# Kernel optimization log

Measured on AMD Instinct MI355X. Metric: run time of the kernel, lower is better.

## Reference

```python
import jax, jax.numpy as jnp
import numpy as np

BN_EPS = 1e-5

def _batchnorm(h, gamma, beta):
    # PyTorch BatchNorm1d in training mode: biased batch statistics over dim 0
    mu = jnp.mean(h, axis=0)
    var = jnp.mean((h - mu) ** 2, axis=0)
    return (h - mu) * jax.lax.rsqrt(var + BN_EPS) * gamma + beta


def setup_inputs() -> dict:
    key = jax.random.key(0)
    ks = jax.random.split(key, 8)
    N, E, D = 50000, 800000, 128
    x = jax.random.normal(ks[0], (N, D), dtype=jnp.float32)
    edge_index = jax.random.randint(ks[1], (2, E), 0, N, dtype=jnp.int64)
    s1 = 1.0 / np.sqrt(D)
    W1 = jax.random.uniform(ks[2], (D, D), jnp.float32, -s1, s1)
    b1 = jax.random.uniform(ks[3], (D,), jnp.float32, -s1, s1)
    W2 = jax.random.uniform(ks[4], (D, D), jnp.float32, -s1, s1)
    b2 = jax.random.uniform(ks[5], (D,), jnp.float32, -s1, s1)
    g1 = jnp.ones((D,), jnp.float32); beta1 = jnp.zeros((D,), jnp.float32)
    g2 = jnp.ones((D,), jnp.float32); beta2 = jnp.zeros((D,), jnp.float32)
    eps = jnp.array([0.1], jnp.float32)
    return {"x": x, "edge_index": edge_index, "eps": eps,
            "W1": W1, "b1": b1, "g1": g1, "beta1": beta1,
            "W2": W2, "b2": b2, "g2": g2, "beta2": beta2}


def reference(x, edge_index, eps, W1, b1, g1, beta1, W2, b2, g2, beta2):
    src, dst = edge_index[0], edge_index[1]
    N = x.shape[0]
    # gather by src, scatter-add to dst
    aggr = jax.ops.segment_sum(x[src], dst, num_segments=N)
    out = (1.0 + eps) * x + aggr  # eps broadcast (shape [1])
    h = jax.nn.relu(_batchnorm(out @ W1 + b1, g1, beta1))
    h = jax.nn.relu(_batchnorm(h @ W2 + b2, g2, beta2))
    return h
```

## Files before the change

### kernel.cpp

```cpp
#include <hip/hip_runtime.h>

#define D 128
#define FB 4096
#define GCAP 1024

typedef __attribute__((ext_vector_type(8))) short short8;
typedef __attribute__((ext_vector_type(4))) float f32x4;

static __device__ __forceinline__ unsigned short f2bf(float f) {
    union { float f; unsigned u; } v; v.f = f;
    unsigned r = v.u + 0x7FFF + ((v.u >> 16) & 1);
    return (unsigned short)(r >> 16);
}

static __device__ __forceinline__ float2 bfpair2f(unsigned p) {
    union { unsigned u; float f; } a, b;
    a.u = (p & 0xFFFFu) << 16;
    b.u = p & 0xFFFF0000u;
    return make_float2(a.f, b.f);
}

__global__ __launch_bounds__(256) void prep_kernel(
    const float4* __restrict__ x4, uint2* __restrict__ xh, int xtotal,
    const float* __restrict__ W1, const float* __restrict__ W2,
    unsigned short* __restrict__ Wf1, unsigned short* __restrict__ Wf2,
    float* __restrict__ stats, int* __restrict__ bucketCount,
    int* __restrict__ bar, unsigned short* __restrict__ zrow, int xblocks)
{
    if (blockIdx.x < (unsigned)xblocks) {
        int i = blockIdx.x * 256 + threadIdx.x;
        if (i >= xtotal) return;
        float4 v = x4[i];
        uint2 o;
        o.x = (unsigned)f2bf(v.x) | ((unsigned)f2bf(v.y) << 16);
        o.y = (unsigned)f2bf(v.z) | ((unsigned)f2bf(v.w) << 16);
        xh[i] = o;
    } else if (blockIdx.x < (unsigned)(xblocks + 128)) {
        int idx = (blockIdx.x - xblocks) * 256 + threadIdx.x;
        const float* W = (idx < 16384) ? W1 : W2;
        unsigned short* Wf = (idx < 16384) ? Wf1 : Wf2;
        int e = idx & 16383;
        int j = e & 7, lane = (e >> 3) & 63, ckk = e >> 9;
        int ct = ckk & 7, kk = ckk >> 3;
        int k = kk * 32 + (lane >> 4) * 8 + j;
        int n = ct * 16 + (lane & 15);
        Wf[e] = f2bf(W[k * 128 + n]);
    } else {
        int t = threadIdx.x;
        stats[t] = 0.f; stats[t + 256] = 0.f;
        bucketCount[t] = 0; bucketCount[t + 256] = 0;
        if (t < 128) zrow[t] = 0;
        if (t < 4) bar[t] = 0;
    }
}

__global__ __launch_bounds__(256) void bucket_hist_kernel(
    const int* __restrict__ ei, int E, int NB, int* __restrict__ bucketCount)
{
    __shared__ int hist[512];
    int tid = threadIdx.x;
    for (int i = tid; i < NB; i += 256) hist[i] = 0;
    __syncthreads();
    int b0 = blockIdx.x * FB;
    int lim = min(FB, E - b0);
    for (int i = tid; i < lim; i += 256)
        atomicAdd(&hist[ei[E + b0 + i] >> 7], 1);
    __syncthreads();
    for (int i = tid; i < NB; i += 256)
        if (hist[i]) atomicAdd(&bucketCount[i], hist[i]);
}

__global__ __launch_bounds__(256) void scanfill_kernel(
    const int* __restrict__ ei, int E, int NB,
    const int* __restrict__ bucketCount,
    int* __restrict__ bucketBase, int* __restrict__ bucketCursor,
    int* __restrict__ flag, unsigned* __restrict__ rec)
{
    int tid = threadIdx.x;
    if (blockIdx.x == 0) {
        __shared__ int sm[256];
        int i0 = 2 * tid, i1 = 2 * tid + 1;
        int c0 = (i0 < NB) ? bucketCount[i0] : 0;
        int c1 = (i1 < NB) ? bucketCount[i1] : 0;
        int t = c0 + c1;
        sm[tid] = t;
        __syncthreads();
        #pragma unroll
        for (int off = 1; off < 256; off <<= 1) {
            int u = (tid >= off) ? sm[tid - off] : 0;
            __syncthreads();
            sm[tid] += u;
            __syncthreads();
        }
        int ex = sm[tid] - t;
        if (i0 < NB) { bucketBase[i0] = ex;      bucketCursor[i0] = ex; }
        if (i1 < NB) { bucketBase[i1] = ex + c0; bucketCursor[i1] = ex + c0; }
        if (tid == 0) bucketBase[NB] = E;
        __threadfence();
        __syncthreads();
        if (tid == 0)
            __hip_atomic_store(flag, 1, __ATOMIC_RELEASE, __HIP_MEMORY_SCOPE_AGENT);
    } else {
        __shared__ int hist[512], base[512];
        int b0 = (blockIdx.x - 1) * FB;
        for (int i = tid; i < NB; i += 256) hist[i] = 0;
        __syncthreads();
        int lim = min(FB, E - b0);
        for (int i = tid; i < lim; i += 256)
            atomicAdd(&hist[ei[E + b0 + i] >> 7], 1);
        __syncthreads();
        if (tid == 0) {
            while (__hip_atomic_load(flag, __ATOMIC_ACQUIRE, __HIP_MEMORY_SCOPE_AGENT) == 0)
                __builtin_amdgcn_s_sleep(2);
        }
        __syncthreads();
        for (int i = tid; i < NB; i += 256) {
            int c = hist[i];
            base[i] = c ? atomicAdd(&bucketCursor[i], c) : 0;
            hist[i] = 0;
        }
        __syncthreads();
        for (int i = tid; i < lim; i += 256) {
            int e = b0 + i;
            int dst = ei[E + e], src = ei[e];
            int bk = dst >> 7;
            int r = atomicAdd(&hist[bk], 1);
            rec[base[bk] + r] = ((unsigned)src << 7) | (unsigned)(dst & 127);
        }
    }
}

__global__ __launch_bounds__(256) void bucket_gather_kernel(
    const unsigned* __restrict__ xh, const unsigned* __restrict__ rec,
    const int* __restrict__ bucketBase, const float* __restrict__ epsp,
    unsigned* __restrict__ h0, int N, int zrow)
{
    int bk = blockIdx.x >> 2;
    int sub = blockIdx.x & 3;
    int tid = threadIdx.x;
    int d0 = (bk << 7) + (sub << 5);

    __shared__ int cnts[32], rnk[32], offs[33];
    __shared__ int slist[GCAP];

    if (tid < 32) { cnts[tid] = 0; rnk[tid] = 0; }
    __syncthreads();

    int lo = bucketBase[bk], hi = bucketBase[bk + 1];
    for (int i = lo + tid; i < hi; i += 256) {
        unsigned r = rec[i];
        int dl = r & 127;
        if ((dl >> 5) == sub) atomicAdd(&cnts[dl & 31], 1);
    }
    __syncthreads();
    if (tid == 0) {
        int run = 0;
        #pragma unroll
        for (int i = 0; i < 32; ++i) { offs[i] = run; run += cnts[i]; }
        offs[32] = run;
    }
    __syncthreads();
    for (int i = lo + tid; i < hi; i += 256) {
        unsigned r = rec[i];
        int dl = r & 127;
        if ((dl >> 5) == sub) {
            int d5 = dl & 31;
            int rk = atomicAdd(&rnk[d5], 1);
            int pos = offs[d5] + rk;
            if (pos < GCAP) slist[pos] = (int)(r >> 7);
        }
    }
    __syncthreads();

    int wv = tid >> 6, lane = tid & 63;
    float epsv = 1.0f + __ldg(epsp);

    #pragma unroll 1
    for (int jj = 0; jj < 4; ++jj) {
        int dA = d0 + wv * 8 + jj * 2;
        int dB = dA + 1;
        int vA = (dA < N), vB = (dB < N);
        int iA = offs[(dA - d0)];
        int eA = offs[(dA - d0) + 1];
        int iB = vB ? offs[(dB - d0)] : 0;
        int eB = vB ? offs[(dB - d0) + 1] : 0;
        if (iA > GCAP) iA = GCAP;
        if (eA > GCAP) eA = GCAP;
        if (iB > GCAP) iB = GCAP;
        if (eB > GCAP) eB = GCAP;
        if (!vA) { iA = 0; eA = 0; }

        float2 xvA = bfpair2f(xh[(size_t)(vA ? dA : 0) * 64 + lane]);
        float2 xvB = bfpair2f(xh[(size_t)(vB ? dB : 0) * 64 + lane]);
        float axA = epsv * xvA.x, ayA = epsv * xvA.y;
        float axB = epsv * xvB.x, ayB = epsv * xvB.y;

        int iters = (eA - iA) > (eB - iB) ? (eA - iA) : (eB - iB);
        for (int it = 0; it < iters; it += 8) {
            unsigned pvA[8], pvB[8];
            #pragma unroll
            for (int k = 0; k < 8; ++k) {
                int idxA = (iA + k < eA) ? slist[iA + k] : zrow;
                int idxB = (iB + k < eB) ? slist[iB + k] : zrow;
                pvA[k] = xh[(size_t)idxA * 64 + lane];
                pvB[k] = xh[(size_t)idxB * 64 + lane];
            }
            #pragma unroll
            for (int k = 0; k < 8; ++k) {
                float2 a = bfpair2f(pvA[k]);
                float2 b = bfpair2f(pvB[k]);
                axA += a.x; ayA += a.y;
                axB += b.x; ayB += b.y;
            }
            iA += 8; iB += 8;
        }
        if (vA) h0[(size_t)dA * 64 + lane] =
            (unsigned)f2bf(axA) | ((unsigned)f2bf(ayA) << 16);
        if (vB) h0[(size_t)dB * 64 + lane] =
            (unsigned)f2bf(axB) | ((unsigned)f2bf(ayB) << 16);
    }
}

__global__ __launch_bounds__(256) void gemm_bn_mfma_kernel(
    const unsigned short* __restrict__ a_bf,
    const float* __restrict__ stat_in, const float* __restrict__ gamma,
    const float* __restrict__ beta, float invN,
    const unsigned short* __restrict__ Wf, const float* __restrict__ bias,
    unsigned short* __restrict__ zout,
    float* __restrict__ stat_sum, float* __restrict__ stat_sq,
    int N, int mode)
{
    __shared__ unsigned short Wl[16384];
    __shared__ float part[1024];
    __shared__ float scf[128], shf[128];

    int tid = threadIdx.x;
    {
        float4* dst = (float4*)Wl;
        const float4* srcp = (const float4*)Wf;
        #pragma unroll
        for (int i = 0; i < 8; ++i) dst[tid + i * 256] = srcp[tid + i * 256];
    }
    if (mode == 1 && tid < 128) {
        float mean = stat_in[tid] * invN;
        float var  = stat_in[128 + tid] * invN - mean * mean;
        float sv = gamma[tid] * rsqrtf(var + 1e-5f);
        scf[tid] = sv;
        shf[tid] = fmaf(-mean, sv, beta[tid]);
    }
    __syncthreads();

    int w = tid >> 6, lane = tid & 63, q = lane >> 4, n16 = lane & 15;
    int rowb = blockIdx.x * 64 + w * 16;
    int m = rowb + n16;
    int mc = (m < N) ? m : (N - 1);
    const unsigned short* arow = a_bf + (size_t)mc * D;

    f32x4 acc[8];
    #pragma unroll
    for (int ct = 0; ct < 8; ++ct) acc[ct] = (f32x4){0.f, 0.f, 0.f, 0.f};

    #pragma unroll
    for (int kk = 0; kk < 4; ++kk) {
        int c = kk * 32 + q * 8;
        short8 af;
        if (mode == 0) {
            af = *(const short8*)(arow + c);
        } else {
            uint4 rw = *(const uint4*)(arow + c);
            float2 p0 = bfpair2f(rw.x), p1 = bfpair2f(rw.y);
            float2 p2 = bfpair2f(rw.z), p3 = bfpair2f(rw.w);
            p0.x = fmaxf(fmaf(p0.x, scf[c + 0], shf[c + 0]), 0.f);
            p0.y = fmaxf(fmaf(p0.y, scf[c + 1], shf[c + 1]), 0.f);
            p1.x = fmaxf(fmaf(p1.x, scf[c + 2], shf[c + 2]), 0.f);
            p1.y = fmaxf(fmaf(p1.y, scf[c + 3], shf[c + 3]), 0.f);
            p2.x = fmaxf(fmaf(p2.x, scf[c + 4], shf[c + 4]), 0.f);
            p2.y = fmaxf(fmaf(p2.y, scf[c + 5], shf[c + 5]), 0.f);
            p3.x = fmaxf(fmaf(p3.x, scf[c + 6], shf[c + 6]), 0.f);
            p3.y = fmaxf(fmaf(p3.y, scf[c + 7], shf[c + 7]), 0.f);
            af[0] = (short)f2bf(p0.x); af[1] = (short)f2bf(p0.y);
            af[2] = (short)f2bf(p1.x); af[3] = (short)f2bf(p1.y);
            af[4] = (short)f2bf(p2.x); af[5] = (short)f2bf(p2.y);
            af[6] = (short)f2bf(p3.x); af[7] = (short)f2bf(p3.y);
        }
        #pragma unroll
        for (int ct = 0; ct < 8; ++ct) {
            short8 bf = *(const short8*)&Wl[(((kk * 8 + ct) * 64) + lane) * 8];
            acc[ct] = __builtin_amdgcn_mfma_f32_16x16x32_bf16(af, bf, acc[ct], 0, 0, 0);
        }
    }

    #pragma unroll
    for (int ct = 0; ct < 8; ++ct) {
        int col = ct * 16 + n16;
        float bv = __ldg(bias + col);
        float s = 0.f, qs = 0.f;
        #pragma unroll
        for (int reg = 0; reg < 4; ++reg) {
            int row = rowb + q * 4 + reg;
            float v = acc[ct][reg] + bv;
            if (row < N) {
                zout[(size_t)row * D + col] = f2bf(v);
                s += v;
                qs = fmaf(v, v, qs);
            }
        }
        s  += __shfl_xor(s, 16, 64);
        s  += __shfl_xor(s, 32, 64);
        qs += __shfl_xor(qs, 16, 64);
        qs += __shfl_xor(qs, 32, 64);
        if (lane < 16) {
            part[w * 128 + col] = s;
            part[512 + w * 128 + col] = qs;
        }
    }
    __syncthreads();

    if (tid < 128) {
        float s  = part[tid] + part[128 + tid] + part[256 + tid] + part[384 + tid];
        float qq = part[512 + tid] + part[640 + tid] + part[768 + tid] + part[896 + tid];
        atomicAdd(&stat_sum[tid], s);
        atomicAdd(&stat_sq[tid], qq);
    }
}

__global__ __launch_bounds__(256) void bn_relu_kernel(
    const uint2* __restrict__ z2, float4* __restrict__ out,
    const float* __restrict__ stat2, const float* __restrict__ gamma,
    const float* __restrict__ beta, float invN, int total4)
{
    __shared__ float sf[128], tf[128];
    int tid = threadIdx.x;
    if (tid < 128) {
        float mean = stat2[tid] * invN;
        float var  = stat2[128 + tid] * invN - mean * mean;
        float sv = gamma[tid] * rsqrtf(var + 1e-5f);
        sf[tid] = sv;
        tf[tid] = fmaf(-mean, sv, beta[tid]);
    }
    __syncthreads();

    int i = blockIdx.x * 256 + tid;
    if (i >= total4) return;
    uint2 zp = z2[i];
    float2 v01 = bfpair2f(zp.x);
    float2 v23 = bfpair2f(zp.y);
    int c = (i & 31) * 4;
    float4 o;
    o.x = fmaxf(fmaf(v01.x, sf[c + 0], tf[c + 0]), 0.f);
    o.y = fmaxf(fmaf(v01.y, sf[c + 1], tf[c + 1]), 0.f);
    o.z = fmaxf(fmaf(v23.x, sf[c + 2], tf[c + 2]), 0.f);
    o.w = fmaxf(fmaf(v23.y, sf[c + 3], tf[c + 3]), 0.f);
    out[i] = o;
}

extern "C" void kernel_launch(void* const* d_in, const int* in_sizes, int n_in,
                              void* d_out, int out_size, void* d_ws, size_t ws_size,
                              hipStream_t stream)
{
    const float* x   = (const float*)d_in[0];
    const int*   ei  = (const int*)d_in[1];
    const float* eps = (const float*)d_in[2];
    const float* W1  = (const float*)d_in[3];
    const float* b1  = (const float*)d_in[4];
    const float* g1  = (const float*)d_in[5];
    const float* be1 = (const float*)d_in[6];
    const float* W2  = (const float*)d_in[7];
    const float* b2  = (const float*)d_in[8];
    const float* g2  = (const float*)d_in[9];
    const float* be2 = (const float*)d_in[10];

    int N = in_sizes[0] / D;
    int E = in_sizes[1] / 2;
    size_t ND = (size_t)N * D;
    int NB = (N + 127) >> 7;

    unsigned short* xh  = (unsigned short*)d_ws;
    unsigned short* z1  = xh;
    unsigned short* region2 = xh + ND + 128;
    unsigned* rec       = (unsigned*)region2;
    unsigned short* z2  = region2;
    float* stats        = (float*)(region2 + ND);
    int* bucketCount    = (int*)(stats + 512);
    int* bucketBase     = bucketCount + 512;
    int* bucketCursor   = bucketBase + 513;
    int* bar            = bucketCursor + 512;
    unsigned short* Wf1 = (unsigned short*)(bar + 4);
    unsigned short* Wf2 = Wf1 + 16384;

    float* sum1 = stats + 0,   *sq1 = stats + 128;
    float* sum2 = stats + 256, *sq2 = stats + 384;
    unsigned short* h0 = (unsigned short*)d_out;

    int xtotal = N * 32;
    int xblocks = (xtotal + 255) / 256;
    prep_kernel<<<xblocks + 129, 256, 0, stream>>>(
        (const float4*)x, (uint2*)xh, xtotal, W1, W2, Wf1, Wf2,
        stats, bucketCount, bar, xh + ND, xblocks);

    int fblocks = (E + FB - 1) / FB;
    bucket_hist_kernel<<<fblocks, 256, 0, stream>>>(ei, E, NB, bucketCount);
    scanfill_kernel<<<fblocks + 1, 256, 0, stream>>>(
        ei, E, NB, bucketCount, bucketBase, bucketCursor, bar, rec);
    bucket_gather_kernel<<<NB * 4, 256, 0, stream>>>(
        (const unsigned*)xh, rec, bucketBase, eps, (unsigned*)h0, N, N);

    int gblocks = (N + 63) / 64;
    gemm_bn_mfma_kernel<<<gblocks, 256, 0, stream>>>(
        h0, nullptr, nullptr, nullptr, 0.f,
        Wf1, b1, z1, sum1, sq1, N, 0);
    gemm_bn_mfma_kernel<<<gblocks, 256, 0, stream>>>(
        z1, sum1, g1, be1, 1.0f / N,
        Wf2, b2, z2, sum2, sq2, N, 1);
    bn_relu_kernel<<<(N * 32 + 255) / 256, 256, 0, stream>>>(
        (const uint2*)z2, (float4*)d_out, sum2, g2, be2, 1.0f / N, N * 32);
}
```

Measured before the change: 230.5 us.

## Fuse bucket histogram into prep kernel and widen gather loads to 8 bytes

```diff
diff --git a/kernel.cpp b/kernel.cpp
--- a/kernel.cpp
+++ b/kernel.cpp
@@ -24,11 +24,13 @@
     const float4* __restrict__ x4, uint2* __restrict__ xh, int xtotal,
     const float* __restrict__ W1, const float* __restrict__ W2,
     unsigned short* __restrict__ Wf1, unsigned short* __restrict__ Wf2,
-    float* __restrict__ stats, int* __restrict__ bucketCount,
-    int* __restrict__ bar, unsigned short* __restrict__ zrow, int xblocks)
-{
+    const int* __restrict__ ei, int E, int NB, int* __restrict__ hg,
+    float* __restrict__ stats, int* __restrict__ bar,
+    unsigned short* __restrict__ zrow, int xblocks, int fblocks)
+{
+    int tid = threadIdx.x;
     if (blockIdx.x < (unsigned)xblocks) {
-        int i = blockIdx.x * 256 + threadIdx.x;
+        int i = blockIdx.x * 256 + tid;
         if (i >= xtotal) return;
         float4 v = x4[i];
         uint2 o;
@@ -36,7 +38,7 @@
         o.y = (unsigned)f2bf(v.z) | ((unsigned)f2bf(v.w) << 16);
         xh[i] = o;
     } else if (blockIdx.x < (unsigned)(xblocks + 128)) {
-        int idx = (blockIdx.x - xblocks) * 256 + threadIdx.x;
+        int idx = (blockIdx.x - xblocks) * 256 + tid;
         const float* W = (idx < 16384) ? W1 : W2;
         unsigned short* Wf = (idx < 16384) ? Wf1 : Wf2;
         int e = idx & 16383;
@@ -45,43 +47,41 @@
         int k = kk * 32 + (lane >> 4) * 8 + j;
         int n = ct * 16 + (lane & 15);
         Wf[e] = f2bf(W[k * 128 + n]);
+    } else if (blockIdx.x < (unsigned)(xblocks + 128 + fblocks)) {
+        int b = blockIdx.x - (xblocks + 128);
+        __shared__ int hist[512];
+        for (int i = tid; i < 512; i += 256) hist[i] = 0;
+        __syncthreads();
+        int b0 = b * FB;
+        int lim = min(FB, E - b0);
+        for (int i = tid; i < lim; i += 256)
+            atomicAdd(&hist[ei[E + b0 + i] >> 7], 1);
+        __syncthreads();
+        for (int i = tid; i < 512; i += 256) hg[b * 512 + i] = hist[i];
     } else {
-        int t = threadIdx.x;
-        stats[t] = 0.f; stats[t + 256] = 0.f;
-        bucketCount[t] = 0; bucketCount[t + 256] = 0;
-        if (t < 128) zrow[t] = 0;
-        if (t < 4) bar[t] = 0;
-    }
-}
-
-__global__ __launch_bounds__(256) void bucket_hist_kernel(
-    const int* __restrict__ ei, int E, int NB, int* __restrict__ bucketCount)
-{
-    __shared__ int hist[512];
-    int tid = threadIdx.x;
-    for (int i = tid; i < NB; i += 256) hist[i] = 0;
-    __syncthreads();
-    int b0 = blockIdx.x * FB;
-    int lim = min(FB, E - b0);
-    for (int i = tid; i < lim; i += 256)
-        atomicAdd(&hist[ei[E + b0 + i] >> 7], 1);
-    __syncthreads();
-    for (int i = tid; i < NB; i += 256)
-        if (hist[i]) atomicAdd(&bucketCount[i], hist[i]);
+        stats[tid] = 0.f; stats[tid + 256] = 0.f;
+        if (tid < 128) zrow[tid] = 0;
+        if (tid < 4) bar[tid] = 0;
+    }
 }
 
 __global__ __launch_bounds__(256) void scanfill_kernel(
-    const int* __restrict__ ei, int E, int NB,
-    const int* __restrict__ bucketCount,
+    const int* __restrict__ ei, int E, int NB, int fblocks,
+    const int* __restrict__ hg,
     int* __restrict__ bucketBase, int* __restrict__ bucketCursor,
     int* __restrict__ flag, unsigned* __restrict__ rec)
 {
     int tid = threadIdx.x;
     if (blockIdx.x == 0) {
         __shared__ int sm[256];
-        int i0 = 2 * tid, i1 = 2 * tid + 1;
-        int c0 = (i0 < NB) ? bucketCount[i0] : 0;
-        int c1 = (i1 < NB) ? bucketCount[i1] : 0;
+        const int2* hg2 = (const int2*)hg;
+        int c0 = 0, c1 = 0;
+        #pragma unroll 4
+        for (int c = 0; c < fblocks; ++c) {
+            int2 v = hg2[c * 256 + tid];
+            c0 += v.x; c1 += v.y;
+        }
+        int i0 = 2 * tid, i1 = i0 + 1;
         int t = c0 + c1;
         sm[tid] = t;
         __syncthreads();
@@ -131,9 +131,9 @@
 }
 
 __global__ __launch_bounds__(256) void bucket_gather_kernel(
-    const unsigned* __restrict__ xh, const unsigned* __restrict__ rec,
+    const uint2* __restrict__ xh2, const unsigned* __restrict__ rec,
     const int* __restrict__ bucketBase, const float* __restrict__ epsp,
-    unsigned* __restrict__ h0, int N, int zrow)
+    uint2* __restrict__ h0, int N, int zrow)
 {
     int bk = blockIdx.x >> 2;
     int sub = blockIdx.x & 3;
@@ -173,6 +173,7 @@
     __syncthreads();
 
     int wv = tid >> 6, lane = tid & 63;
+    int half = lane >> 5, sl = lane & 31;
     float epsv = 1.0f + __ldg(epsp);
 
     #pragma unroll 1
@@ -180,44 +181,70 @@
         int dA = d0 + wv * 8 + jj * 2;
         int dB = dA + 1;
         int vA = (dA < N), vB = (dB < N);
-        int iA = offs[(dA - d0)];
-        int eA = offs[(dA - d0) + 1];
-        int iB = vB ? offs[(dB - d0)] : 0;
-        int eB = vB ? offs[(dB - d0) + 1] : 0;
-        if (iA > GCAP) iA = GCAP;
+        int a_i = dA - d0, b_i = dB - d0;
+        int iA0 = offs[a_i],            eA = offs[a_i + 1];
+        int iB0 = vB ? offs[b_i] : 0,   eB = vB ? offs[b_i + 1] : 0;
+        if (iA0 > GCAP) iA0 = GCAP;
         if (eA > GCAP) eA = GCAP;
-        if (iB > GCAP) iB = GCAP;
+        if (iB0 > GCAP) iB0 = GCAP;
         if (eB > GCAP) eB = GCAP;
-        if (!vA) { iA = 0; eA = 0; }
-
-        float2 xvA = bfpair2f(xh[(size_t)(vA ? dA : 0) * 64 + lane]);
-        float2 xvB = bfpair2f(xh[(size_t)(vB ? dB : 0) * 64 + lane]);
-        float axA = epsv * xvA.x, ayA = epsv * xvA.y;
-        float axB = epsv * xvB.x, ayB = epsv * xvB.y;
-
-        int iters = (eA - iA) > (eB - iB) ? (eA - iA) : (eB - iB);
+        if (!vA) { iA0 = 0; eA = 0; }
+
+        int dInit = half ? (vB ? dB : 0) : (vA ? dA : 0);
+        uint2 xv = xh2[(size_t)dInit * 32 + sl];
+        float2 p01 = bfpair2f(xv.x), p23 = bfpair2f(xv.y);
+        float mA = (half == 0 && vA) ? epsv : 0.f;
+        float mB = (half == 1 && vB) ? epsv : 0.f;
+        float4 accA = make_float4(mA * p01.x, mA * p01.y, mA * p23.x, mA * p23.y);
+        float4 accB = make_float4(mB * p01.x, mB * p01.y, mB * p23.x, mB * p23.y);
+
+        int lenA = eA - iA0, lenB = eB - iB0;
+        int iters = lenA > lenB ? lenA : lenB;
+        int iA = iA0 + half, iB = iB0 + half;
         for (int it = 0; it < iters; it += 8) {
-            unsigned pvA[8], pvB[8];
+            uint2 pv[8];
             #pragma unroll
-            for (int k = 0; k < 8; ++k) {
-                int idxA = (iA + k < eA) ? slist[iA + k] : zrow;
-                int idxB = (iB + k < eB) ? slist[iB + k] : zrow;
-                pvA[k] = xh[(size_t)idxA * 64 + lane];
-                pvB[k] = xh[(size_t)idxB * 64 + lane];
+            for (int k = 0; k < 4; ++k) {
+                int pA = iA + 2 * k;
+                int idxA = (pA < eA) ? slist[pA] : zrow;
+                pv[k] = xh2[(size_t)idxA * 32 + sl];
             }
             #pragma unroll
-            for (int k = 0; k < 8; ++k) {
-                float2 a = bfpair2f(pvA[k]);
-                float2 b = bfpair2f(pvB[k]);
-                axA += a.x; ayA += a.y;
-                axB += b.x; ayB += b.y;
+            for (int k = 0; k < 4; ++k) {
+                int pB = iB + 2 * k;
+                int idxB = (pB < eB) ? slist[pB] : zrow;
+                pv[4 + k] = xh2[(size_t)idxB * 32 + sl];
+            }
+            #pragma unroll
+            for (int k = 0; k < 4; ++k) {
+                float2 q01 = bfpair2f(pv[k].x), q23 = bfpair2f(pv[k].y);
+                accA.x += q01.x; accA.y += q01.y;
+                accA.z += q23.x; accA.w += q23.y;
+                float2 r01 = bfpair2f(pv[4 + k].x), r23 = bfpair2f(pv[4 + k].y);
+                accB.x += r01.x; accB.y += r01.y;
+                accB.z += r23.x; accB.w += r23.y;
             }
             iA += 8; iB += 8;
         }
-        if (vA) h0[(size_t)dA * 64 + lane] =
-            (unsigned)f2bf(axA) | ((unsigned)f2bf(ayA) << 16);
-        if (vB) h0[(size_t)dB * 64 + lane] =
-            (unsigned)f2bf(axB) | ((unsigned)f2bf(ayB) << 16);
+
+        accA.x += __shfl_xor(accA.x, 32, 64);
+        accA.y += __shfl_xor(accA.y, 32, 64);
+        accA.z += __shfl_xor(accA.z, 32, 64);
+        accA.w += __shfl_xor(accA.w, 32, 64);
+        accB.x += __shfl_xor(accB.x, 32, 64);
+        accB.y += __shfl_xor(accB.y, 32, 64);
+        accB.z += __shfl_xor(accB.z, 32, 64);
+        accB.w += __shfl_xor(accB.w, 32, 64);
+
+        int dOut = half ? dB : dA;
+        int vOut = half ? vB : vA;
+        float4 ac = half ? accB : accA;
+        if (vOut) {
+            uint2 o;
+            o.x = (unsigned)f2bf(ac.x) | ((unsigned)f2bf(ac.y) << 16);
+            o.y = (unsigned)f2bf(ac.z) | ((unsigned)f2bf(ac.w) << 16);
+            h0[(size_t)dOut * 32 + sl] = o;
+        }
     }
 }
 
@@ -374,6 +401,7 @@
     int E = in_sizes[1] / 2;
     size_t ND = (size_t)N * D;
     int NB = (N + 127) >> 7;
+    int fblocks = (E + FB - 1) / FB;
 
     unsigned short* xh  = (unsigned short*)d_ws;
     unsigned short* z1  = xh;
@@ -381,12 +409,12 @@
     unsigned* rec       = (unsigned*)region2;
     unsigned short* z2  = region2;
     float* stats        = (float*)(region2 + ND);
-    int* bucketCount    = (int*)(stats + 512);
-    int* bucketBase     = bucketCount + 512;
+    int* bucketBase     = (int*)(stats + 512);
     int* bucketCursor   = bucketBase + 513;
     int* bar            = bucketCursor + 512;
     unsigned short* Wf1 = (unsigned short*)(bar + 4);
     unsigned short* Wf2 = Wf1 + 16384;
+    int* hg             = (int*)(Wf2 + 16384);
 
     float* sum1 = stats + 0,   *sq1 = stats + 128;
     float* sum2 = stats + 256, *sq2 = stats + 384;
@@ -394,16 +422,14 @@
 
     int xtotal = N * 32;
     int xblocks = (xtotal + 255) / 256;
-    prep_kernel<<<xblocks + 129, 256, 0, stream>>>(
+    prep_kernel<<<xblocks + 128 + fblocks + 1, 256, 0, stream>>>(
         (const float4*)x, (uint2*)xh, xtotal, W1, W2, Wf1, Wf2,
-        stats, bucketCount, bar, xh + ND, xblocks);
-
-    int fblocks = (E + FB - 1) / FB;
-    bucket_hist_kernel<<<fblocks, 256, 0, stream>>>(ei, E, NB, bucketCount);
+        ei, E, NB, hg, stats, bar, xh + ND, xblocks, fblocks);
+
     scanfill_kernel<<<fblocks + 1, 256, 0, stream>>>(
-        ei, E, NB, bucketCount, bucketBase, bucketCursor, bar, rec);
+        ei, E, NB, fblocks, hg, bucketBase, bucketCursor, bar, rec);
     bucket_gather_kernel<<<NB * 4, 256, 0, stream>>>(
-        (const unsigned*)xh, rec, bucketBase, eps, (unsigned*)h0, N, N);
+        (const uint2*)xh, rec, bucketBase, eps, (uint2*)h0, N, N);
 
     int gblocks = (N + 63) / 64;
     gemm_bn_mfma_kernel<<<gblocks, 256, 0, stream>>>(
```

Measured after the change: 262.2 us. 13.8% more time.
